# Optimization experiments

Measured on AMD Instinct MI355X. Metric: run time of the kernel, lower is better.

The kernel has to match this reference:

```python
import jax, jax.numpy as jnp
import numpy as np


def setup_inputs() -> dict:
    key = jax.random.key(0)
    ks = jax.random.split(key, 5)
    B, S, D, F = 4, 2048, 1024, 4096
    scale_w1 = 1.0 / np.sqrt(D)
    scale_w2 = 1.0 / np.sqrt(F)
    return {
        "hidden_states": jax.random.normal(ks[0], (B, S, D), dtype=jnp.float32),
        "W1": jax.random.normal(ks[1], (F, D), dtype=jnp.float32) * scale_w1,
        "b1": jax.random.normal(ks[2], (F,), dtype=jnp.float32) * 0.02,
        "W2": jax.random.normal(ks[3], (D, F), dtype=jnp.float32) * scale_w2,
        "b2": jax.random.normal(ks[4], (D,), dtype=jnp.float32) * 0.02,
    }


def _sigmoid_poly(h):
    # cubic polynomial sigmoid approximation: 0.5 + 0.25*h - 0.0208*h^3
    h2 = h * h
    h3 = h2 * h
    return 0.5 + 0.25 * h + (-0.0208) * h3


def reference(hidden_states, W1, b1, W2, b2):
    # secure linear projection == plain affine: x @ W.T + b
    h = jnp.einsum("bsd,fd->bsf", hidden_states, W1) + b1  # [B,S,F]
    sw = h * _sigmoid_poly(h)                               # swish via poly sigmoid
    out = jnp.einsum("bsf,df->bsd", sw, W2) + b2            # [B,S,D]
    return out
```

## Files before the change

### kernel.cpp

```cpp
#include <hip/hip_runtime.h>
#include <hip/hip_bf16.h>

typedef __bf16 bf16_t;
typedef __bf16 bf16x8 __attribute__((ext_vector_type(8)));
typedef float f32x4 __attribute__((ext_vector_type(4)));

typedef const __attribute__((address_space(3))) bf16_t* lds_cptr;

__global__ __launch_bounds__(256) void cast3_f32_to_bf16(
    const float* __restrict__ a, bf16_t* __restrict__ ao, int na8,
    const float* __restrict__ b, bf16_t* __restrict__ bo, int nb8,
    const float* __restrict__ c, bf16_t* __restrict__ co, int nc8) {
  int i = blockIdx.x * blockDim.x + threadIdx.x;
  const float* in;
  bf16_t* out;
  int j;
  if (i < na8) {
    in = a; out = ao; j = i;
  } else if (i < na8 + nb8) {
    in = b; out = bo; j = i - na8;
  } else if (i < na8 + nb8 + nc8) {
    in = c; out = co; j = i - na8 - nb8;
  } else {
    return;
  }
  const float4* in4 = (const float4*)in;
  float4 f0 = in4[2 * j];
  float4 f1 = in4[2 * j + 1];
  bf16x8 o;
  o[0] = (bf16_t)f0.x; o[1] = (bf16_t)f0.y;
  o[2] = (bf16_t)f0.z; o[3] = (bf16_t)f0.w;
  o[4] = (bf16_t)f1.x; o[5] = (bf16_t)f1.y;
  o[6] = (bf16_t)f1.z; o[7] = (bf16_t)f1.w;
  ((bf16x8*)out)[j] = o;
}

__device__ __forceinline__ void gload_lds16(const bf16_t* g, bf16_t* l) {
  __builtin_amdgcn_global_load_lds(
      (const __attribute__((address_space(1))) void*)g,
      (__attribute__((address_space(3))) void*)l,
      16, 0, 0);
}

template <int N>
__device__ __forceinline__ void vmwait() {
  asm volatile("s_waitcnt vmcnt(%0)" :: "i"(N));
}

template <int N>
__device__ __forceinline__ void lgkmwait() {
  asm volatile("s_waitcnt lgkmcnt(%0)" :: "i"(N));
}

template <int I, int E>
__device__ __forceinline__ void ldsr_rng(bf16x8* dst, lds_cptr p) {
  if constexpr (I < E) {
    asm volatile("ds_read_b128 %0, %1 offset:%2"
                 : "=v"(dst[I]) : "v"(p), "i"(I * 1024));
    ldsr_rng<I + 1, E>(dst, p);
  }
}

template <int I, int END, int FR, int FC, int BASE>
__device__ __forceinline__ void mfma_gr(const bf16x8 (&aq)[FR],
                                        const bf16x8 (&bq)[FC],
                                        f32x4 (&acc)[FR][FC]) {
  if constexpr (I < END) {
    lgkmwait<BASE - I>();
    __builtin_amdgcn_sched_barrier(0);
#pragma unroll
    for (int j = 0; j < FC; ++j)
      acc[I][j] = __builtin_amdgcn_mfma_f32_16x16x32_bf16(
          aq[I], bq[j], acc[I][j], 0, 0, 0);
    mfma_gr<I + 1, END, FR, FC, BASE>(aq, bq, acc);
  }
}

#define BODY(bc_, bn_, sw_, AC, BC, AN, BNX)                                  \
  {                                                                           \
    stageA(sw_);                                                              \
    stageB(sw_);                                                              \
    __builtin_amdgcn_sched_barrier(0);                                        \
    __builtin_amdgcn_s_setprio(1);                                            \
    mfma_gr<0, FR / 2, FR, FC, FR - 1>(AC, BC, acc);                          \
    __builtin_amdgcn_s_setprio(0);                                            \
    vmwait<2 * VMN>();                                                        \
    __builtin_amdgcn_sched_barrier(0);                                        \
    lds_cptr paN = sA3 + (bn_) * (256 * 32) + aoff;                           \
    lds_cptr pbN = sB3 + (bn_) * (BN * 32) + boff;                            \
    ldsr_rng<0, FC>(BNX, pbN);                                                \
    ldsr_rng<0, 2>(AN, paN);                                                  \
    __builtin_amdgcn_s_setprio(1);                                            \
    mfma_gr<FR / 2, FR, FR, FC, FR + 5>(AC, BC, acc);                         \
    __builtin_amdgcn_s_setprio(0);                                            \
    ldsr_rng<2, FR>(AN, paN);                                                 \
    __builtin_amdgcn_s_barrier();                                             \
  }

template <int BN, int WM, int WN, bool SWISH>
__global__ __launch_bounds__(512, 2) void gemm_bt8(
    const bf16_t* __restrict__ A, const bf16_t* __restrict__ B,
    const float* __restrict__ bias, void* __restrict__ Cout,
    int M, int N, int K, int XW, int px, int py) {
  constexpr int BM = 256;
  constexpr int WR = BM / WM;
  constexpr int WC = BN / WN;
  constexpr int FR = WR / 16;
  constexpr int FC = WC / 16;
  constexpr int ACALLS = BM / 128;
  constexpr int BCALLS = BN / 128;
  constexpr int VMN = ACALLS + BCALLS;

  const int tid = threadIdx.x;
  const int wave = tid >> 6;
  const int lane = tid & 63;

  const int bid = blockIdx.x;
  const int xcd = bid & 7;
  const int idx = bid >> 3;
  const int cx = xcd % XW;
  const int cy = xcd / XW;
  const int bx = cx * px + idx % px;
  const int by = cy * py + idx / px;
  const int tileM = by * BM;
  const int tileN = bx * BN;

  __shared__ __align__(16) bf16_t sA[4 * 256 * 32];
  __shared__ __align__(16) bf16_t sB[4 * BN * 32];
  lds_cptr sA3 = (lds_cptr)sA;
  lds_cptr sB3 = (lds_cptr)sB;

  const int srow = (wave << 4) + (lane >> 2);
  const int sgc = ((lane & 3) ^ ((lane >> 3) & 3)) << 3;
  const bf16_t* gA = A + (size_t)(tileM + srow) * K + sgc;
  const bf16_t* gB = B + (size_t)(tileN + srow) * K + sgc;
  bf16_t* lA = sA + (wave << 9);
  bf16_t* lB = sB + (wave << 9);

  auto stageA = [&](int s) {
    bf16_t* l = lA + (s & 3) * (256 * 32);
    const bf16_t* g = gA + s * 32;
#pragma unroll
    for (int c = 0; c < ACALLS; ++c)
      gload_lds16(g + (size_t)(c * 128) * K, l + c * 128 * 32);
  };
  auto stageB = [&](int s) {
    bf16_t* l = lB + (s & 3) * (BN * 32);
    const bf16_t* g = gB + s * 32;
#pragma unroll
    for (int c = 0; c < BCALLS; ++c)
      gload_lds16(g + (size_t)(c * 128) * K, l + c * 128 * 32);
  };

  const int wr = wave / WN;
  const int wc = wave % WN;
  const int fr = lane & 15;
  const int pc = (lane >> 4) ^ ((fr >> 1) & 3);
  const int aoff = (wr * WR + fr) * 32 + pc * 8;
  const int boff = (wc * WC + fr) * 32 + pc * 8;

  f32x4 acc[FR][FC] = {};
  bf16x8 aR0[FR], bR0[FC], aR1[FR], bR1[FC];

  const int NS = K >> 5;

  stageA(0); stageB(0);
  stageA(1); stageB(1);
  stageA(2); stageB(2);
  vmwait<2 * VMN>();
  __builtin_amdgcn_s_barrier();
  __builtin_amdgcn_sched_barrier(0);
  ldsr_rng<0, FC>(bR0, sB3 + boff);
  ldsr_rng<0, FR>(aR0, sA3 + aoff);

  for (int os = 0; os < NS; os += 4) {
    int w0 = os + 3;     if (w0 >= NS) w0 -= NS;
    int w1 = os + 4;     if (w1 >= NS) w1 -= NS;
    int w2 = os + 5;     if (w2 >= NS) w2 -= NS;
    int w3 = os + 6;     if (w3 >= NS) w3 -= NS;
    BODY(0, 1, w0, aR0, bR0, aR1, bR1)
    BODY(1, 2, w1, aR1, bR1, aR0, bR0)
    BODY(2, 3, w2, aR0, bR0, aR1, bR1)
    BODY(3, 0, w3, aR1, bR1, aR0, bR0)
  }
  lgkmwait<0>();
  __builtin_amdgcn_sched_barrier(0);

  const int cRow0 = tileM + wr * WR + ((lane >> 4) << 2);
  const int cCol0 = tileN + wc * WC + (lane & 15);
  float bv[FC];
#pragma unroll
  for (int j = 0; j < FC; ++j) bv[j] = bias[cCol0 + j * 16];
#pragma unroll
  for (int i = 0; i < FR; ++i) {
#pragma unroll
    for (int r = 0; r < 4; ++r) {
      const size_t row = (size_t)(cRow0 + i * 16 + r);
#pragma unroll
      for (int j = 0; j < FC; ++j) {
        float h = acc[i][j][r] + bv[j];
        if constexpr (SWISH) {
          float h3 = h * h * h;
          float sw = h * (0.5f + 0.25f * h - 0.0208f * h3);
          ((bf16_t*)Cout)[row * N + cCol0 + j * 16] = (bf16_t)sw;
        } else {
          ((float*)Cout)[row * N + cCol0 + j * 16] = h;
        }
      }
    }
  }
}

extern "C" void kernel_launch(void* const* d_in, const int* in_sizes, int n_in,
                              void* d_out, int out_size, void* d_ws,
                              size_t ws_size, hipStream_t stream) {
  const float* X  = (const float*)d_in[0];
  const float* W1 = (const float*)d_in[1];
  const float* b1 = (const float*)d_in[2];
  const float* W2 = (const float*)d_in[3];
  const float* b2 = (const float*)d_in[4];
  float* out = (float*)d_out;

  const int F = in_sizes[2];
  const int D = in_sizes[4];
  const int M = in_sizes[0] / D;

  bf16_t* Xb  = (bf16_t*)d_ws;
  bf16_t* W1b = Xb + (size_t)M * D;
  bf16_t* W2b = W1b + (size_t)F * D;
  bf16_t* SW  = W2b + (size_t)D * F;

  const int nX = (M * D) / 8, nW1 = (F * D) / 8, nW2 = (D * F) / 8;
  const int nTot = nX + nW1 + nW2;
  cast3_f32_to_bf16<<<(nTot + 255) / 256, 256, 0, stream>>>(
      X, Xb, nX, W1, W1b, nW1, W2, W2b, nW2);

  {
    const int gx = F / 256, gy = M / 256;
    const int XW = 2, XH = 4;
    const int px = gx / XW, py = gy / XH;
    gemm_bt8<256, 2, 4, true><<<gx * gy, 512, 0, stream>>>(
        Xb, W1b, b1, (void*)SW, M, F, D, XW, px, py);
  }

  {
    const int gx = D / 128, gy = M / 256;
    const int XW = 1, XH = 8;
    const int px = gx / XW, py = gy / XH;
    gemm_bt8<128, 4, 2, false><<<gx * gy, 512, 0, stream>>>(
        SW, W2b, b2, (void*)out, M, D, F, XW, px, py);
  }
}
```

Measured before the change: 245.8 us.

## Restructure GEMM main loop into barrier-separated load/compute phases with smaller register fragments

Replaces the double-buffered register ping-pong (interleaving LDS reads for the next k-step with MFMAs of the current one) with explicit phases. Each phase issues its global-to-LDS stage, reads 4x4 fragments from LDS, waits, then runs a block of 16 MFMAs between workgroup barriers. For the first GEMM (FR=8) it splits into two row-half phases, reusing the B fragments and staggering the A and B stages. This cuts register use (one fragment set instead of two) but serialises LDS reads and compute within a wave and adds barriers, counting on the other resident waves to hide the latency. The cast kernel also switches from 8 to 4 elements per thread.

```diff
diff --git a/kernel.cpp b/kernel.cpp
--- a/kernel.cpp
+++ b/kernel.cpp
@@ -3,36 +3,33 @@
 
 typedef __bf16 bf16_t;
 typedef __bf16 bf16x8 __attribute__((ext_vector_type(8)));
+typedef __bf16 bf16x4v __attribute__((ext_vector_type(4)));
 typedef float f32x4 __attribute__((ext_vector_type(4)));
 
 typedef const __attribute__((address_space(3))) bf16_t* lds_cptr;
 
 __global__ __launch_bounds__(256) void cast3_f32_to_bf16(
-    const float* __restrict__ a, bf16_t* __restrict__ ao, int na8,
-    const float* __restrict__ b, bf16_t* __restrict__ bo, int nb8,
-    const float* __restrict__ c, bf16_t* __restrict__ co, int nc8) {
+    const float4* __restrict__ a, bf16x4v* __restrict__ ao, int na4,
+    const float4* __restrict__ b, bf16x4v* __restrict__ bo, int nb4,
+    const float4* __restrict__ c, bf16x4v* __restrict__ co, int nc4) {
   int i = blockIdx.x * blockDim.x + threadIdx.x;
-  const float* in;
-  bf16_t* out;
+  const float4* in;
+  bf16x4v* out;
   int j;
-  if (i < na8) {
+  if (i < na4) {
     in = a; out = ao; j = i;
-  } else if (i < na8 + nb8) {
-    in = b; out = bo; j = i - na8;
-  } else if (i < na8 + nb8 + nc8) {
-    in = c; out = co; j = i - na8 - nb8;
+  } else if (i < na4 + nb4) {
+    in = b; out = bo; j = i - na4;
+  } else if (i < na4 + nb4 + nc4) {
+    in = c; out = co; j = i - na4 - nb4;
   } else {
     return;
   }
-  const float4* in4 = (const float4*)in;
-  float4 f0 = in4[2 * j];
-  float4 f1 = in4[2 * j + 1];
-  bf16x8 o;
-  o[0] = (bf16_t)f0.x; o[1] = (bf16_t)f0.y;
-  o[2] = (bf16_t)f0.z; o[3] = (bf16_t)f0.w;
-  o[4] = (bf16_t)f1.x; o[5] = (bf16_t)f1.y;
-  o[6] = (bf16_t)f1.z; o[7] = (bf16_t)f1.w;
-  ((bf16x8*)out)[j] = o;
+  float4 f = in[j];
+  bf16x4v o;
+  o[0] = (bf16_t)f.x; o[1] = (bf16_t)f.y;
+  o[2] = (bf16_t)f.z; o[3] = (bf16_t)f.w;
+  out[j] = o;
 }
 
 __device__ __forceinline__ void gload_lds16(const bf16_t* g, bf16_t* l) {
@@ -52,53 +49,87 @@
   asm volatile("s_waitcnt lgkmcnt(%0)" :: "i"(N));
 }
 
-template <int I, int E>
-__device__ __forceinline__ void ldsr_rng(bf16x8* dst, lds_cptr p) {
-  if constexpr (I < E) {
+template <int I, int N, int BASE>
+__device__ __forceinline__ void ldsr(bf16x8* dst, lds_cptr p) {
+  if constexpr (I < N) {
     asm volatile("ds_read_b128 %0, %1 offset:%2"
-                 : "=v"(dst[I]) : "v"(p), "i"(I * 1024));
-    ldsr_rng<I + 1, E>(dst, p);
-  }
-}
-
-template <int I, int END, int FR, int FC, int BASE>
-__device__ __forceinline__ void mfma_gr(const bf16x8 (&aq)[FR],
-                                        const bf16x8 (&bq)[FC],
-                                        f32x4 (&acc)[FR][FC]) {
-  if constexpr (I < END) {
-    lgkmwait<BASE - I>();
-    __builtin_amdgcn_sched_barrier(0);
-#pragma unroll
-    for (int j = 0; j < FC; ++j)
-      acc[I][j] = __builtin_amdgcn_mfma_f32_16x16x32_bf16(
-          aq[I], bq[j], acc[I][j], 0, 0, 0);
-    mfma_gr<I + 1, END, FR, FC, BASE>(aq, bq, acc);
-  }
-}
-
-#define BODY(bc_, bn_, sw_, AC, BC, AN, BNX)                                  \
+                 : "=v"(dst[I]) : "v"(p), "i"(BASE + I * 1024));
+    ldsr<I + 1, N, BASE>(dst, p);
+  }
+}
+
+template <int R0, int FR>
+__device__ __forceinline__ void mfma_clu(const bf16x8 (&aq)[4],
+                                         const bf16x8 (&bq)[4],
+                                         f32x4 (&acc)[FR][4]) {
+#pragma unroll
+  for (int i = 0; i < 4; ++i)
+#pragma unroll
+    for (int j = 0; j < 4; ++j)
+      acc[R0 + i][j] = __builtin_amdgcn_mfma_f32_16x16x32_bf16(
+          aq[i], bq[j], acc[R0 + i][j], 0, 0, 0);
+}
+
+#define PHASE_R0(b_, sw_)                                                     \
+  {                                                                           \
+    stageA(sw_);                                                              \
+    lds_cptr pa = sA3 + (b_) * (256 * 32) + aoff;                             \
+    lds_cptr pb = sB3 + (b_) * (BN * 32) + boff;                              \
+    ldsr<0, 4, 0>(bq, pb);                                                    \
+    ldsr<0, 4, 0>(aq, pa);                                                    \
+    vmwait<LEAVE>();                                                          \
+    __builtin_amdgcn_s_barrier();                                             \
+    lgkmwait<0>();                                                            \
+    __builtin_amdgcn_sched_barrier(0);                                        \
+    __builtin_amdgcn_s_setprio(1);                                            \
+    mfma_clu<0, FR>(aq, bq, acc);                                             \
+    __builtin_amdgcn_s_setprio(0);                                            \
+    __builtin_amdgcn_s_barrier();                                             \
+  }
+
+#define PHASE_R1(b_, sw_)                                                     \
+  {                                                                           \
+    stageB(sw_);                                                              \
+    lds_cptr pa = sA3 + (b_) * (256 * 32) + aoff;                             \
+    ldsr<0, 4, 4 * 1024>(aq, pa);                                             \
+    vmwait<LEAVE>();                                                          \
+    __builtin_amdgcn_s_barrier();                                             \
+    lgkmwait<0>();                                                            \
+    __builtin_amdgcn_sched_barrier(0);                                        \
+    __builtin_amdgcn_s_setprio(1);                                            \
+    mfma_clu<4, FR>(aq, bq, acc);                                             \
+    __builtin_amdgcn_s_setprio(0);                                            \
+    __builtin_amdgcn_s_barrier();                                             \
+  }
+
+#define PHASE_G2(b_, sw_)                                                     \
   {                                                                           \
     stageA(sw_);                                                              \
     stageB(sw_);                                                              \
+    lds_cptr pa = sA3 + (b_) * (256 * 32) + aoff;                             \
+    lds_cptr pb = sB3 + (b_) * (BN * 32) + boff;                              \
+    ldsr<0, 4, 0>(bq, pb);                                                    \
+    ldsr<0, 4, 0>(aq, pa);                                                    \
+    vmwait<LEAVE>();                                                          \
+    __builtin_amdgcn_s_barrier();                                             \
+    lgkmwait<0>();                                                            \
     __builtin_amdgcn_sched_barrier(0);                                        \
     __builtin_amdgcn_s_setprio(1);                                            \
-    mfma_gr<0, FR / 2, FR, FC, FR - 1>(AC, BC, acc);                          \
+    mfma_clu<0, FR>(aq, bq, acc);                                             \
     __builtin_amdgcn_s_setprio(0);                                            \
-    vmwait<2 * VMN>();                                                        \
-    __builtin_amdgcn_sched_barrier(0);                                        \
-    lds_cptr paN = sA3 + (bn_) * (256 * 32) + aoff;                           \
-    lds_cptr pbN = sB3 + (bn_) * (BN * 32) + boff;                            \
-    ldsr_rng<0, FC>(BNX, pbN);                                                \
-    ldsr_rng<0, 2>(AN, paN);                                                  \
-    __builtin_amdgcn_s_setprio(1);                                            \
-    mfma_gr<FR / 2, FR, FR, FC, FR + 5>(AC, BC, acc);                         \
-    __builtin_amdgcn_s_setprio(0);                                            \
-    ldsr_rng<2, FR>(AN, paN);                                                 \
-    __builtin_amdgcn_s_barrier();                                             \
+    __builtin_amdgcn_s_barrier();                                             \
+  }
+
+#define SUBTILE(b_, sw_)                                                      \
+  if constexpr (RH == 2) {                                                    \
+    PHASE_R0(b_, sw_)                                                         \
+    PHASE_R1(b_, sw_)                                                         \
+  } else {                                                                    \
+    PHASE_G2(b_, sw_)                                                         \
   }
 
 template <int BN, int WM, int WN, bool SWISH>
-__global__ __launch_bounds__(512, 2) void gemm_bt8(
+__global__ __launch_bounds__(512, 2) void gemm_fp(
     const bf16_t* __restrict__ A, const bf16_t* __restrict__ B,
     const float* __restrict__ bias, void* __restrict__ Cout,
     int M, int N, int K, int XW, int px, int py) {
@@ -106,10 +137,10 @@
   constexpr int WR = BM / WM;
   constexpr int WC = BN / WN;
   constexpr int FR = WR / 16;
-  constexpr int FC = WC / 16;
+  constexpr int RH = FR / 4;
   constexpr int ACALLS = BM / 128;
   constexpr int BCALLS = BN / 128;
-  constexpr int VMN = ACALLS + BCALLS;
+  constexpr int LEAVE = (RH == 2) ? 4 : 6;
 
   const int tid = threadIdx.x;
   const int wave = tid >> 6;
@@ -159,45 +190,42 @@
   const int aoff = (wr * WR + fr) * 32 + pc * 8;
   const int boff = (wc * WC + fr) * 32 + pc * 8;
 
-  f32x4 acc[FR][FC] = {};
-  bf16x8 aR0[FR], bR0[FC], aR1[FR], bR1[FC];
+  f32x4 acc[FR][4] = {};
+  bf16x8 aq[4], bq[4];
 
   const int NS = K >> 5;
 
   stageA(0); stageB(0);
   stageA(1); stageB(1);
   stageA(2); stageB(2);
-  vmwait<2 * VMN>();
+  vmwait<LEAVE>();
   __builtin_amdgcn_s_barrier();
-  __builtin_amdgcn_sched_barrier(0);
-  ldsr_rng<0, FC>(bR0, sB3 + boff);
-  ldsr_rng<0, FR>(aR0, sA3 + aoff);
 
   for (int os = 0; os < NS; os += 4) {
     int w0 = os + 3;     if (w0 >= NS) w0 -= NS;
     int w1 = os + 4;     if (w1 >= NS) w1 -= NS;
     int w2 = os + 5;     if (w2 >= NS) w2 -= NS;
     int w3 = os + 6;     if (w3 >= NS) w3 -= NS;
-    BODY(0, 1, w0, aR0, bR0, aR1, bR1)
-    BODY(1, 2, w1, aR1, bR1, aR0, bR0)
-    BODY(2, 3, w2, aR0, bR0, aR1, bR1)
-    BODY(3, 0, w3, aR1, bR1, aR0, bR0)
+    SUBTILE(0, w0)
+    SUBTILE(1, w1)
+    SUBTILE(2, w2)
+    SUBTILE(3, w3)
   }
   lgkmwait<0>();
   __builtin_amdgcn_sched_barrier(0);
 
   const int cRow0 = tileM + wr * WR + ((lane >> 4) << 2);
   const int cCol0 = tileN + wc * WC + (lane & 15);
-  float bv[FC];
-#pragma unroll
-  for (int j = 0; j < FC; ++j) bv[j] = bias[cCol0 + j * 16];
+  float bv[4];
+#pragma unroll
+  for (int j = 0; j < 4; ++j) bv[j] = bias[cCol0 + j * 16];
 #pragma unroll
   for (int i = 0; i < FR; ++i) {
 #pragma unroll
     for (int r = 0; r < 4; ++r) {
       const size_t row = (size_t)(cRow0 + i * 16 + r);
 #pragma unroll
-      for (int j = 0; j < FC; ++j) {
+      for (int j = 0; j < 4; ++j) {
         float h = acc[i][j][r] + bv[j];
         if constexpr (SWISH) {
           float h3 = h * h * h;
@@ -230,16 +258,18 @@
   bf16_t* W2b = W1b + (size_t)F * D;
   bf16_t* SW  = W2b + (size_t)D * F;
 
-  const int nX = (M * D) / 8, nW1 = (F * D) / 8, nW2 = (D * F) / 8;
+  const int nX = (M * D) / 4, nW1 = (F * D) / 4, nW2 = (D * F) / 4;
   const int nTot = nX + nW1 + nW2;
   cast3_f32_to_bf16<<<(nTot + 255) / 256, 256, 0, stream>>>(
-      X, Xb, nX, W1, W1b, nW1, W2, W2b, nW2);
+      (const float4*)X, (bf16x4v*)Xb, nX,
+      (const float4*)W1, (bf16x4v*)W1b, nW1,
+      (const float4*)W2, (bf16x4v*)W2b, nW2);
 
   {
     const int gx = F / 256, gy = M / 256;
     const int XW = 2, XH = 4;
     const int px = gx / XW, py = gy / XH;
-    gemm_bt8<256, 2, 4, true><<<gx * gy, 512, 0, stream>>>(
+    gemm_fp<256, 2, 4, true><<<gx * gy, 512, 0, stream>>>(
         Xb, W1b, b1, (void*)SW, M, F, D, XW, px, py);
   }
 
@@ -247,7 +277,7 @@
     const int gx = D / 128, gy = M / 256;
     const int XW = 1, XH = 8;
     const int px = gx / XW, py = gy / XH;
-    gemm_bt8<128, 4, 2, false><<<gx * gy, 512, 0, stream>>>(
+    gemm_fp<128, 4, 2, false><<<gx * gy, 512, 0, stream>>>(
         SW, W2b, b2, (void*)out, M, D, F, XW, px, py);
   }
 }
```

Result: no change. 246.6 us (+0.3%).
